# Optimization experiments

Measured on AMD Instinct MI355X. Metric: run time of the kernel, lower is better.

Reference implementation:

```python
import jax, jax.numpy as jnp
import numpy as np

B, N, IN_FT, OUT_FT = 256, 512, 64, 64


def setup_inputs() -> dict:
    key = jax.random.key(0)
    k1, k2, k3 = jax.random.split(key, 3)
    seq = jax.random.normal(k1, (B, N, IN_FT), dtype=jnp.float32)
    adj = jax.random.uniform(k2, (B, N, N), dtype=jnp.float32)
    # Xavier-uniform linear weight [out_ft, in_ft]
    limit = float(np.sqrt(6.0 / (IN_FT + OUT_FT)))
    W = jax.random.uniform(k3, (OUT_FT, IN_FT), dtype=jnp.float32, minval=-limit, maxval=limit)
    bias = jnp.zeros((OUT_FT,), dtype=jnp.float32)  # bias.data.fill_(0.0)
    alpha = jnp.asarray(0.25, dtype=jnp.float32)    # PReLU default single param
    return {"seq": seq, "adj": adj, "W": W, "bias": bias, "alpha": alpha}


def reference(seq, adj, W, bias, alpha):
    # fc: seq @ W.T  -> [B, N, out_ft]
    seq_fts = jnp.einsum('bnf,of->bno', seq, W)
    # dense batched adjacency aggregation: adj @ seq_fts -> [B, N, out_ft]
    out = jnp.einsum('bnm,bmo->bno', adj, seq_fts)
    out = out + bias
    # PReLU with shared alpha
    return jnp.where(out >= 0, out, alpha * out)
```

## Files before the change

### kernel.cpp

```cpp
#include <hip/hip_runtime.h>
#include <hip/hip_bf16.h>


#define BATCH 256
#define NTOK  512
#define INF   64
#define OUTF  64

typedef __attribute__((ext_vector_type(8))) __bf16 bf16x8;
typedef __attribute__((ext_vector_type(4))) __bf16 bf16x4;
typedef __attribute__((ext_vector_type(4))) float  f32x4;

typedef const __attribute__((address_space(1))) char GChar;
typedef __attribute__((address_space(3))) char LChar;

__device__ __forceinline__ bf16x8 load_cvt8(const float* __restrict__ p) {
    float4 lo = *(const float4*)p;
    float4 hi = *(const float4*)(p + 4);
    bf16x8 r;
    r[0] = (__bf16)lo.x; r[1] = (__bf16)lo.y; r[2] = (__bf16)lo.z; r[3] = (__bf16)lo.w;
    r[4] = (__bf16)hi.x; r[5] = (__bf16)hi.y; r[6] = (__bf16)hi.z; r[7] = (__bf16)hi.w;
    return r;
}

__device__ __forceinline__ bf16x8 pack8(float4 lo, float4 hi) {
    bf16x8 r;
    r[0] = (__bf16)lo.x; r[1] = (__bf16)lo.y; r[2] = (__bf16)lo.z; r[3] = (__bf16)lo.w;
    r[4] = (__bf16)hi.x; r[5] = (__bf16)hi.y; r[6] = (__bf16)hi.z; r[7] = (__bf16)hi.w;
    return r;
}

__global__ __launch_bounds__(1024, 4) void GCN_fused_kernel(
        const float* __restrict__ seq, const float* __restrict__ adj,
        const float* __restrict__ W, const float* __restrict__ bias,
        const float* __restrict__ alpha_p, float* __restrict__ out) {
    __shared__ float smem[32768];

    int b    = blockIdx.x;
    int tid  = threadIdx.x;
    int wave = tid >> 6;
    int lane = tid & 63;
    int row16 = lane & 15;
    int g     = lane >> 4;
    int c     = wave & 3;
    int r     = wave >> 2;
    int rs    = row16 & 7;

    __bf16* sft = (__bf16*)smem;

    {
        int mb = wave * 32;
        bf16x8 wf[4][2];
#pragma unroll
        for (int nt = 0; nt < 4; ++nt)
#pragma unroll
            for (int ks = 0; ks < 2; ++ks)
                wf[nt][ks] = load_cvt8(W + (size_t)(nt * 16 + row16) * INF + ks * 32 + g * 8);

#pragma unroll
        for (int mt = 0; mt < 2; ++mt) {
            f32x4 pa[4] = {};
#pragma unroll
            for (int ks = 0; ks < 2; ++ks) {
                bf16x8 af = load_cvt8(seq + ((size_t)b * NTOK + mb + mt * 16 + row16) * INF + ks * 32 + g * 8);
#pragma unroll
                for (int nt = 0; nt < 4; ++nt)
                    pa[nt] = __builtin_amdgcn_mfma_f32_16x16x32_bf16(af, wf[nt][ks], pa[nt], 0, 0, 0);
            }
#pragma unroll
            for (int nt = 0; nt < 4; ++nt) {
                int o    = nt * 16 + row16;
                int ktok = mb + mt * 16 + g * 4;
                int sw   = (ktok >> 3) ^ (o & 7);
                bf16x4 v;
                v[0] = (__bf16)pa[nt][0]; v[1] = (__bf16)pa[nt][1];
                v[2] = (__bf16)pa[nt][2]; v[3] = (__bf16)pa[nt][3];
                *(bf16x4*)((char*)sft + (size_t)o * 1024 + sw * 16 + (ktok & 7) * 2) = v;
            }
        }
    }
    __syncthreads();

    int orow = c * 16 + row16;
    bf16x8 bbr[16];
#pragma unroll
    for (int t = 0; t < 16; ++t) {
        int sw = ((t << 2) + g) ^ rs;
        bbr[t] = *(const bf16x8*)((const char*)sft + (size_t)orow * 1024 + sw * 16);
    }
    __syncthreads();

    float bv     = bias[orow];
    float alphav = alpha_p[0];
    f32x4 acc[8];
#pragma unroll
    for (int mt = 0; mt < 8; ++mt) { acc[mt][0] = bv; acc[mt][1] = bv; acc[mt][2] = bv; acc[mt][3] = bv; }

    asm volatile("s_waitcnt vmcnt(0)" ::: "memory");
    __builtin_amdgcn_sched_barrier(0);

    int rl = lane >> 3;
    int sl = (lane & 7) ^ rl;
    const float* gsrc = adj + ((size_t)b * NTOK + r * 128 + rl) * NTOK + sl * 4;
    float* gb0 = smem + (size_t)(r * 2 + 0) * 4096;
    float* gb1 = smem + (size_t)(r * 2 + 1) * 4096;

#define STAGE(dstf, kcc) do {                                                  \
    _Pragma("unroll")                                                          \
    for (int i_ = 0; i_ < 4; ++i_) {                                           \
        int idx_ = c * 4 + i_;                                                 \
        __builtin_amdgcn_global_load_lds(                                      \
            (GChar*)(gsrc + (size_t)idx_ * 8 * NTOK + (kcc)),                  \
            (LChar*)((dstf) + idx_ * 256), 16, 0, 0);                          \
    }                                                                          \
} while (0)

    STAGE(gb0, 0);

#pragma unroll
    for (int it = 0; it < 16; ++it) {
        int kc = it * 32;
        float* cur = (it & 1) ? gb1 : gb0;
        float* nxt = (it & 1) ? gb0 : gb1;

        if (it > 0) {
            __builtin_amdgcn_sched_barrier(0);
            __builtin_amdgcn_s_barrier();
            __builtin_amdgcn_sched_barrier(0);
        }
        if (it < 15) STAGE(nxt, kc + 32);
        __builtin_amdgcn_sched_barrier(0);
        if (it < 15) asm volatile("s_waitcnt vmcnt(4)" ::: "memory");
        else         asm volatile("s_waitcnt vmcnt(0)" ::: "memory");
        __builtin_amdgcn_sched_barrier(0);
        __builtin_amdgcn_s_barrier();
        __builtin_amdgcn_sched_barrier(0);

#pragma unroll
        for (int mt = 0; mt < 8; ++mt) {
            int rloc = mt * 16 + row16;
            int s0   = (g * 2) ^ rs;
            float4 f0 = *(const float4*)(cur + rloc * 32 + s0 * 4);
            float4 f1 = *(const float4*)(cur + rloc * 32 + (s0 ^ 1) * 4);
            bf16x8 a = pack8(f0, f1);
            acc[mt] = __builtin_amdgcn_mfma_f32_16x16x32_bf16(a, bbr[it], acc[mt], 0, 0, 0);
        }
    }
#undef STAGE

#pragma unroll
    for (int mt = 0; mt < 8; ++mt) {
        int m = r * 128 + mt * 16 + g * 4;
        float* op = out + ((size_t)b * NTOK + m) * OUTF + orow;
#pragma unroll
        for (int j = 0; j < 4; ++j) {
            float v = acc[mt][j];
            op[(size_t)j * OUTF] = (v >= 0.f) ? v : alphav * v;
        }
    }
}

extern "C" void kernel_launch(void* const* d_in, const int* in_sizes, int n_in,
                              void* d_out, int out_size, void* d_ws, size_t ws_size,
                              hipStream_t stream) {
    const float* seq   = (const float*)d_in[0];
    const float* adj   = (const float*)d_in[1];
    const float* W     = (const float*)d_in[2];
    const float* bias  = (const float*)d_in[3];
    const float* alpha = (const float*)d_in[4];
    float* out = (float*)d_out;

    GCN_fused_kernel<<<dim3(BATCH), dim3(1024), 0, stream>>>(seq, adj, W, bias, alpha, out);
}
```

Baseline: 76.19 us.

## Restructure aggregation to stream full-width adj row blocks with 512-thread blocks

Switches from K-chunked streaming (each wave accumulating 8 row tiles over 16 K chunks) to row-block streaming: each iteration loads 32 full rows of adj (all 512 columns) into LDS, computes a full-K MFMA reduction for one 16-row tile per wave, and writes the output immediately. The block shrinks to 512 threads, and the first adj prefetch is issued before the seq@W projection so the loads overlap it. This reduces accumulator register pressure and spreads stores across the loop. The cost is fewer waves per block to hide latency and a loop that is no longer unrolled.

```diff
diff --git a/kernel.cpp b/kernel.cpp
--- a/kernel.cpp
+++ b/kernel.cpp
@@ -30,7 +30,7 @@
     return r;
 }
 
-__global__ __launch_bounds__(1024, 4) void GCN_fused_kernel(
+__global__ __launch_bounds__(512, 2) void GCN_fused_kernel(
         const float* __restrict__ seq, const float* __restrict__ adj,
         const float* __restrict__ W, const float* __restrict__ bias,
         const float* __restrict__ alpha_p, float* __restrict__ out) {
@@ -43,13 +43,32 @@
     int row16 = lane & 15;
     int g     = lane >> 4;
     int c     = wave & 3;
-    int r     = wave >> 2;
+    int mt    = wave >> 2;
     int rs    = row16 & 7;
 
     __bf16* sft = (__bf16*)smem;
+    float* buf0 = smem + 16384;
+    float* buf1 = smem;
+
+    const float* gadj = adj + (size_t)b * NTOK * NTOK;
+
+#define STAGE(dstf, rbase) do {                                                \
+    _Pragma("unroll")                                                          \
+    for (int i_ = 0; i_ < 8; ++i_) {                                           \
+        int idx_  = wave * 8 + i_;                                             \
+        int row_  = idx_ >> 1;                                                 \
+        int half_ = idx_ & 1;                                                  \
+        __builtin_amdgcn_global_load_lds(                                      \
+            (GChar*)(gadj + (size_t)((rbase) + row_) * NTOK + half_ * 256      \
+                     + (lane ^ (row_ & 7)) * 4),                               \
+            (LChar*)((dstf) + idx_ * 256), 16, 0, 0);                          \
+    }                                                                          \
+} while (0)
+
+    STAGE(buf0, 0);
 
     {
-        int mb = wave * 32;
+        int mb = wave * 64;
         bf16x8 wf[4][2];
 #pragma unroll
         for (int nt = 0; nt < 4; ++nt)
@@ -58,11 +77,11 @@
                 wf[nt][ks] = load_cvt8(W + (size_t)(nt * 16 + row16) * INF + ks * 32 + g * 8);
 
 #pragma unroll
-        for (int mt = 0; mt < 2; ++mt) {
+        for (int mt2 = 0; mt2 < 4; ++mt2) {
             f32x4 pa[4] = {};
 #pragma unroll
             for (int ks = 0; ks < 2; ++ks) {
-                bf16x8 af = load_cvt8(seq + ((size_t)b * NTOK + mb + mt * 16 + row16) * INF + ks * 32 + g * 8);
+                bf16x8 af = load_cvt8(seq + ((size_t)b * NTOK + mb + mt2 * 16 + row16) * INF + ks * 32 + g * 8);
 #pragma unroll
                 for (int nt = 0; nt < 4; ++nt)
                     pa[nt] = __builtin_amdgcn_mfma_f32_16x16x32_bf16(af, wf[nt][ks], pa[nt], 0, 0, 0);
@@ -70,7 +89,7 @@
 #pragma unroll
             for (int nt = 0; nt < 4; ++nt) {
                 int o    = nt * 16 + row16;
-                int ktok = mb + mt * 16 + g * 4;
+                int ktok = mb + mt2 * 16 + g * 4;
                 int sw   = (ktok >> 3) ^ (o & 7);
                 bf16x4 v;
                 v[0] = (__bf16)pa[nt][0]; v[1] = (__bf16)pa[nt][1];
@@ -79,9 +98,11 @@
             }
         }
     }
+    int orow     = c * 16 + row16;
+    float bv     = bias[orow];
+    float alphav = alpha_p[0];
     __syncthreads();
 
-    int orow = c * 16 + row16;
     bf16x8 bbr[16];
 #pragma unroll
     for (int t = 0; t < 16; ++t) {
@@ -90,74 +111,46 @@
     }
     __syncthreads();
 
-    float bv     = bias[orow];
-    float alphav = alpha_p[0];
-    f32x4 acc[8];
-#pragma unroll
-    for (int mt = 0; mt < 8; ++mt) { acc[mt][0] = bv; acc[mt][1] = bv; acc[mt][2] = bv; acc[mt][3] = bv; }
-
-    asm volatile("s_waitcnt vmcnt(0)" ::: "memory");
-    __builtin_amdgcn_sched_barrier(0);
-
-    int rl = lane >> 3;
-    int sl = (lane & 7) ^ rl;
-    const float* gsrc = adj + ((size_t)b * NTOK + r * 128 + rl) * NTOK + sl * 4;
-    float* gb0 = smem + (size_t)(r * 2 + 0) * 4096;
-    float* gb1 = smem + (size_t)(r * 2 + 1) * 4096;
-
-#define STAGE(dstf, kcc) do {                                                  \
-    _Pragma("unroll")                                                          \
-    for (int i_ = 0; i_ < 4; ++i_) {                                           \
-        int idx_ = c * 4 + i_;                                                 \
-        __builtin_amdgcn_global_load_lds(                                      \
-            (GChar*)(gsrc + (size_t)idx_ * 8 * NTOK + (kcc)),                  \
-            (LChar*)((dstf) + idx_ * 256), 16, 0, 0);                          \
-    }                                                                          \
-} while (0)
-
-    STAGE(gb0, 0);
-
-#pragma unroll
+#pragma unroll 1
     for (int it = 0; it < 16; ++it) {
-        int kc = it * 32;
-        float* cur = (it & 1) ? gb1 : gb0;
-        float* nxt = (it & 1) ? gb0 : gb1;
+        float* cur = (it & 1) ? buf1 : buf0;
+        float* nxt = (it & 1) ? buf0 : buf1;
 
         if (it > 0) {
             __builtin_amdgcn_sched_barrier(0);
             __builtin_amdgcn_s_barrier();
             __builtin_amdgcn_sched_barrier(0);
         }
-        if (it < 15) STAGE(nxt, kc + 32);
+        if (it < 15) STAGE(nxt, (it + 1) * 32);
         __builtin_amdgcn_sched_barrier(0);
-        if (it < 15) asm volatile("s_waitcnt vmcnt(4)" ::: "memory");
-        else         asm volatile("s_waitcnt vmcnt(0)" ::: "memory");
+        if (it == 0)       asm volatile("s_waitcnt vmcnt(8)"  ::: "memory");
+        else if (it < 15)  asm volatile("s_waitcnt vmcnt(12)" ::: "memory");
+        else               asm volatile("s_waitcnt vmcnt(4)"  ::: "memory");
         __builtin_amdgcn_sched_barrier(0);
         __builtin_amdgcn_s_barrier();
         __builtin_amdgcn_sched_barrier(0);
 
+        f32x4 acc;
+        acc[0] = bv; acc[1] = bv; acc[2] = bv; acc[3] = bv;
+        int rowb = (mt * 16 + row16) * 512;
 #pragma unroll
-        for (int mt = 0; mt < 8; ++mt) {
-            int rloc = mt * 16 + row16;
-            int s0   = (g * 2) ^ rs;
-            float4 f0 = *(const float4*)(cur + rloc * 32 + s0 * 4);
-            float4 f1 = *(const float4*)(cur + rloc * 32 + (s0 ^ 1) * 4);
+        for (int ks = 0; ks < 16; ++ks) {
+            int s0 = (ks * 8 + g * 2) ^ rs;
+            float4 f0 = *(const float4*)(cur + rowb + s0 * 4);
+            float4 f1 = *(const float4*)(cur + rowb + (s0 ^ 1) * 4);
             bf16x8 a = pack8(f0, f1);
-            acc[mt] = __builtin_amdgcn_mfma_f32_16x16x32_bf16(a, bbr[it], acc[mt], 0, 0, 0);
+            acc = __builtin_amdgcn_mfma_f32_16x16x32_bf16(a, bbr[ks], acc, 0, 0, 0);
+        }
+
+        int m = it * 32 + mt * 16 + g * 4;
+        float* op = out + ((size_t)b * NTOK + m) * OUTF + orow;
+#pragma unroll
+        for (int j = 0; j < 4; ++j) {
+            float v = acc[j];
+            op[(size_t)j * OUTF] = (v >= 0.f) ? v : alphav * v;
         }
     }
 #undef STAGE
-
-#pragma unroll
-    for (int mt = 0; mt < 8; ++mt) {
-        int m = r * 128 + mt * 16 + g * 4;
-        float* op = out + ((size_t)b * NTOK + m) * OUTF + orow;
-#pragma unroll
-        for (int j = 0; j < 4; ++j) {
-            float v = acc[mt][j];
-            op[(size_t)j * OUTF] = (v >= 0.f) ? v : alphav * v;
-        }
-    }
 }
 
 extern "C" void kernel_launch(void* const* d_in, const int* in_sizes, int n_in,
@@ -170,5 +163,5 @@
     const float* alpha = (const float*)d_in[4];
     float* out = (float*)d_out;
 
-    GCN_fused_kernel<<<dim3(BATCH), dim3(1024), 0, stream>>>(seq, adj, W, bias, alpha, out);
+    GCN_fused_kernel<<<dim3(BATCH), dim3(512), 0, stream>>>(seq, adj, W, bias, alpha, out);
 }
```

Result: faster. 72.09 us (-5.4%).
